# Kernel optimization log

Hardware: AMD Instinct MI355X
Metric: run time of the kernel (lower is better)

## Reference

```python
import jax, jax.numpy as jnp
import numpy as np

SCALE = 64.0
MARGIN = 0.35
EPS = 1e-12  # torch F.normalize eps


def _l2norm(a, axis):
    n = jnp.sqrt(jnp.sum(a * a, axis=axis, keepdims=True))
    return a / jnp.maximum(n, EPS)


def setup_inputs() -> dict:
    key = jax.random.key(0)
    k1, k2, k3 = jax.random.split(key, 3)
    B, D, C = 512, 512, 100000
    x = jax.random.normal(k1, (B, D), dtype=jnp.float32)
    gt = jax.random.randint(k2, (B,), 0, C, dtype=jnp.int64)
    # kaiming_normal_ on [C, D]: std = sqrt(2 / fan_in) with fan_in = D
    wt = jax.random.normal(k3, (C, D), dtype=jnp.float32) * np.sqrt(2.0 / D)
    return {"x": x, "gt": gt, "wt": wt}


def reference(x, gt, wt):
    wt_norm = _l2norm(wt, axis=1)          # [C, D]
    x_norm = _l2norm(x, axis=1)            # [B, D]
    cos = jnp.einsum("bd,cd->bc", x_norm, wt_norm)  # [B, C]
    # margin only at target index (avoids materializing one-hot)
    b = jnp.arange(x.shape[0])
    margin_score = cos.at[b, gt].add(-MARGIN)
    logits = SCALE * margin_score
    logp = jax.nn.log_softmax(logits, axis=-1)
    nll = -logp[b, gt]
    return jnp.mean(nll)
```

## Files before the change

kernel.cpp:

```cpp
#include <hip/hip_runtime.h>
#include <hip/hip_bf16.h>

#define DIM 512
#define BATCH 512
#define CCLS 100000
#define BN 128
#define NT 782

typedef __attribute__((ext_vector_type(4))) float f32x4;

__device__ __forceinline__ void async_copy16(const unsigned char* g, unsigned char* l) {
  __builtin_amdgcn_global_load_lds((const __attribute__((address_space(1))) void*)g,
                                   (__attribute__((address_space(3))) void*)l, 16, 0, 0);
}

__global__ __launch_bounds__(256) void xquant(const float* __restrict__ x,
                                              unsigned char* __restrict__ xq,
                                              float* __restrict__ nx) {
  int wave = threadIdx.x >> 6;
  int lane = threadIdx.x & 63;
  int row = blockIdx.x * 4 + wave;
  const float4* src = (const float4*)(x + (size_t)row * DIM);
  float4 v0 = src[2 * lane];
  float4 v1 = src[2 * lane + 1];
  float ss = v0.x*v0.x + v0.y*v0.y + v0.z*v0.z + v0.w*v0.w
           + v1.x*v1.x + v1.y*v1.y + v1.z*v1.z + v1.w*v1.w;
  #pragma unroll
  for (int off = 32; off > 0; off >>= 1) ss += __shfl_xor(ss, off, 64);
  int p0 = __builtin_amdgcn_cvt_pk_fp8_f32(v0.x, v0.y, 0, false);
  p0     = __builtin_amdgcn_cvt_pk_fp8_f32(v0.z, v0.w, p0, true);
  int p1 = __builtin_amdgcn_cvt_pk_fp8_f32(v1.x, v1.y, 0, false);
  p1     = __builtin_amdgcn_cvt_pk_fp8_f32(v1.z, v1.w, p1, true);
  ((int2*)(xq + (size_t)row * DIM))[lane] = make_int2(p0, p1);
  if (lane == 0) nx[row] = fmaxf(sqrtf(ss), 1e-12f);
}

__global__ __launch_bounds__(1024) void cosface_fused(
    const unsigned char* __restrict__ xq,
    const float* __restrict__ wt,
    const int* __restrict__ gt,
    const float* __restrict__ nx,
    float* __restrict__ partial,
    float* __restrict__ tgt) {
  __shared__ __align__(16) unsigned char lds_a[512 * 128];
  __shared__ __align__(16) unsigned char lds_b[BN * 128];
  __shared__ float lds_rowsum[BATCH];
  __shared__ float lds_nx[BATCH];
  __shared__ float lds_nw[BN];
  __shared__ int lds_gt[BATCH];

  const int tid = threadIdx.x;
  const int lane = tid & 63;
  const int w = tid >> 6;
  const int wm = w >> 2;
  const int wn_ = w & 3;
  const int nt = blockIdx.x;

  if (tid < BATCH) {
    lds_rowsum[tid] = 0.f;
    lds_gt[tid] = gt[tid];
    lds_nx[tid] = nx[tid];
  }
  if (tid < BN) lds_nw[tid] = 0.f;

  unsigned int oa[4];
  #pragma unroll
  for (int j = 0; j < 4; ++j) {
    int c = j * 1024 + tid;
    int m = c >> 3;
    int qg = (c & 7) ^ (m & 7);
    oa[j] = (unsigned int)m * DIM + qg * 16;
  }
  const int mB = tid >> 3;
  const int qgB = (tid & 7) ^ (mB & 7);
  int rowB = nt * BN + mB;
  if (rowB >= CCLS) rowB = CCLS - 1;
  const float* wsrc = wt + (size_t)rowB * DIM + qgB * 16;

  f32x4 acc[8][2];
  #pragma unroll
  for (int i = 0; i < 8; ++i)
    #pragma unroll
    for (int j = 0; j < 2; ++j)
      acc[i][j] = (f32x4){0.f, 0.f, 0.f, 0.f};

  const int quad = lane >> 4;
  const int l15 = lane & 15;
  const int sw = l15 & 7;
  __syncthreads();

  for (int kk = 0; kk < 4; ++kk) {
    #pragma unroll
    for (int j = 0; j < 4; ++j)
      async_copy16(xq + oa[j] + kk * 128, &lds_a[(j * 1024 + w * 64) * 16]);
    {
      const float* p = wsrc + kk * 128;
      float4 f0 = *(const float4*)(p);
      float4 f1 = *(const float4*)(p + 4);
      float4 f2 = *(const float4*)(p + 8);
      float4 f3 = *(const float4*)(p + 12);
      f0.x*=16.f; f0.y*=16.f; f0.z*=16.f; f0.w*=16.f;
      f1.x*=16.f; f1.y*=16.f; f1.z*=16.f; f1.w*=16.f;
      f2.x*=16.f; f2.y*=16.f; f2.z*=16.f; f2.w*=16.f;
      f3.x*=16.f; f3.y*=16.f; f3.z*=16.f; f3.w*=16.f;
      float ss = f0.x*f0.x + f0.y*f0.y + f0.z*f0.z + f0.w*f0.w
               + f1.x*f1.x + f1.y*f1.y + f1.z*f1.z + f1.w*f1.w
               + f2.x*f2.x + f2.y*f2.y + f2.z*f2.z + f2.w*f2.w
               + f3.x*f3.x + f3.y*f3.y + f3.z*f3.z + f3.w*f3.w;
      int p0 = __builtin_amdgcn_cvt_pk_fp8_f32(f0.x, f0.y, 0, false);
      p0     = __builtin_amdgcn_cvt_pk_fp8_f32(f0.z, f0.w, p0, true);
      int p1 = __builtin_amdgcn_cvt_pk_fp8_f32(f1.x, f1.y, 0, false);
      p1     = __builtin_amdgcn_cvt_pk_fp8_f32(f1.z, f1.w, p1, true);
      int p2 = __builtin_amdgcn_cvt_pk_fp8_f32(f2.x, f2.y, 0, false);
      p2     = __builtin_amdgcn_cvt_pk_fp8_f32(f2.z, f2.w, p2, true);
      int p3 = __builtin_amdgcn_cvt_pk_fp8_f32(f3.x, f3.y, 0, false);
      p3     = __builtin_amdgcn_cvt_pk_fp8_f32(f3.z, f3.w, p3, true);
      ((int4*)lds_b)[tid] = make_int4(p0, p1, p2, p3);
      ss += __shfl_xor(ss, 1, 64);
      ss += __shfl_xor(ss, 2, 64);
      ss += __shfl_xor(ss, 4, 64);
      if ((lane & 7) == 0) atomicAdd(&lds_nw[mB], ss);
    }
    __syncthreads();

    #pragma unroll
    for (int s = 0; s < 4; ++s) {
      int g = s * 4 + quad;
      int cs = g >> 1;
      int h = (g & 1) * 8;
      long long af[8], bf[2];
      #pragma unroll
      for (int i = 0; i < 8; ++i)
        af[i] = *(const long long*)&lds_a[(wm * 128 + i * 16 + l15) * 128 + ((cs ^ sw) * 16) + h];
      #pragma unroll
      for (int j = 0; j < 2; ++j)
        bf[j] = *(const long long*)&lds_b[(wn_ * 32 + j * 16 + l15) * 128 + ((cs ^ sw) * 16) + h];
      #pragma unroll
      for (int i = 0; i < 8; ++i)
        #pragma unroll
        for (int j = 0; j < 2; ++j)
          acc[i][j] = __builtin_amdgcn_mfma_f32_16x16x32_fp8_fp8(af[i], bf[j], acc[i][j], 0, 0, 0);
    }
    __syncthreads();
  }

  float rnw[2];
  #pragma unroll
  for (int j = 0; j < 2; ++j)
    rnw[j] = 1.0f / fmaxf(sqrtf(lds_nw[wn_ * 32 + j * 16 + l15]), 1e-12f);
  #pragma unroll
  for (int i = 0; i < 8; ++i) {
    #pragma unroll
    for (int reg = 0; reg < 4; ++reg) {
      int m_loc = wm * 128 + i * 16 + quad * 4 + reg;
      int gtm = lds_gt[m_loc];
      float rx = 64.0f / lds_nx[m_loc];
      float s = 0.f;
      #pragma unroll
      for (int j = 0; j < 2; ++j) {
        int n_g = nt * BN + wn_ * 32 + j * 16 + l15;
        float logit = acc[i][j][reg] * rnw[j] * rx;
        if (n_g == gtm) {
          logit -= 64.f * 0.35f;
          tgt[m_loc] = logit;
        }
        if (n_g < CCLS) s += __expf(logit - 64.f);
      }
      #pragma unroll
      for (int off = 1; off < 16; off <<= 1) s += __shfl_xor(s, off, 64);
      if (l15 == 0) atomicAdd(&lds_rowsum[m_loc], s);
    }
  }
  __syncthreads();
  if (tid < BATCH)
    partial[(size_t)tid * NT + nt] = lds_rowsum[tid];
}

__global__ __launch_bounds__(64) void nll_rows(const float* __restrict__ partial,
                                               const float* __restrict__ tgt,
                                               float* __restrict__ nll) {
  int m = blockIdx.x;
  int lane = threadIdx.x;
  const float* row = partial + (size_t)m * NT;
  float s = 0.f;
  for (int t = lane; t < NT; t += 64) s += row[t];
  #pragma unroll
  for (int off = 32; off > 0; off >>= 1) s += __shfl_xor(s, off, 64);
  if (lane == 0) nll[m] = (logf(s) + 64.f) - tgt[m];
}

__global__ __launch_bounds__(512) void reduce_mean(const float* __restrict__ nll,
                                                   float* __restrict__ out) {
  __shared__ float red[BATCH];
  int m = threadIdx.x;
  red[m] = nll[m];
  __syncthreads();
  for (int k = 256; k > 0; k >>= 1) {
    if (m < k) red[m] += red[m + k];
    __syncthreads();
  }
  if (m == 0) out[0] = red[0] * (1.0f / BATCH);
}

extern "C" void kernel_launch(void* const* d_in, const int* in_sizes, int n_in,
                              void* d_out, int out_size, void* d_ws, size_t ws_size,
                              hipStream_t stream) {
  const float* x  = (const float*)d_in[0];
  const int*   gt = (const int*)d_in[1];
  const float* wt = (const float*)d_in[2];
  float* out = (float*)d_out;

  char* ws = (char*)d_ws;
  unsigned char* xq = (unsigned char*)ws;
  float* nx         = (float*)(ws + 262144);
  float* partial    = (float*)(ws + 264192);
  float* tgt        = (float*)(ws + 1865728);
  float* nll        = (float*)(ws + 1867776);

  xquant<<<BATCH / 4, 256, 0, stream>>>(x, xq, nx);
  cosface_fused<<<NT, 1024, 0, stream>>>(xq, wt, gt, nx, partial, tgt);
  nll_rows<<<BATCH, 64, 0, stream>>>(partial, tgt, nll);
  reduce_mean<<<1, BATCH, 0, stream>>>(nll, out);
}
```

Before: 393.7 us.

## Double-buffer K loop with smaller class tiles and register-prefetched weight loads

Class tile width is halved to 64 with 512-thread blocks and a 4-blocks-per-SM launch bound. The K loop now walks 8 steps of 64 bytes with double-buffered LDS for both the fp8 x tile and the quantized weight tile, and global weight loads are prefetched two steps ahead in registers. The per-row weight norm is kept in registers and reduced once at the end, replacing per-step LDS atomics. This aims to overlap the HBM stream of the fp32 weights with MFMA work and raise occupancy. In exchange, the x tile is staged from L2 twice as often in total and the partial-sum array is twice as large.

```diff
diff --git a/kernel.cpp b/kernel.cpp
--- a/kernel.cpp
+++ b/kernel.cpp
@@ -4,8 +4,8 @@
 #define DIM 512
 #define BATCH 512
 #define CCLS 100000
-#define BN 128
-#define NT 782
+#define BN 64
+#define NT 1563
 
 typedef __attribute__((ext_vector_type(4))) float f32x4;
 
@@ -35,47 +35,70 @@
   if (lane == 0) nx[row] = fmaxf(sqrtf(ss), 1e-12f);
 }
 
-__global__ __launch_bounds__(1024) void cosface_fused(
+__global__ __launch_bounds__(512, 4) void cosface_fused(
     const unsigned char* __restrict__ xq,
     const float* __restrict__ wt,
     const int* __restrict__ gt,
     const float* __restrict__ nx,
     float* __restrict__ partial,
     float* __restrict__ tgt) {
-  __shared__ __align__(16) unsigned char lds_a[512 * 128];
-  __shared__ __align__(16) unsigned char lds_b[BN * 128];
-  __shared__ float lds_rowsum[BATCH];
-  __shared__ float lds_nx[BATCH];
+  __shared__ __align__(16) unsigned char lds_a[2][512 * 64];
+  __shared__ __align__(16) unsigned char lds_b[2][BN * 64];
+  __shared__ float lds_rowsum[512];
+  __shared__ float lds_nx[512];
   __shared__ float lds_nw[BN];
-  __shared__ int lds_gt[BATCH];
+  __shared__ int lds_gt[512];
 
   const int tid = threadIdx.x;
   const int lane = tid & 63;
   const int w = tid >> 6;
-  const int wm = w >> 2;
-  const int wn_ = w & 3;
+  const int wm = w >> 1;
+  const int wn_ = w & 1;
   const int nt = blockIdx.x;
 
-  if (tid < BATCH) {
-    lds_rowsum[tid] = 0.f;
-    lds_gt[tid] = gt[tid];
-    lds_nx[tid] = nx[tid];
-  }
-  if (tid < BN) lds_nw[tid] = 0.f;
+  lds_rowsum[tid] = 0.f;
+  lds_gt[tid] = gt[tid];
+  lds_nx[tid] = nx[tid];
 
   unsigned int oa[4];
   #pragma unroll
   for (int j = 0; j < 4; ++j) {
-    int c = j * 1024 + tid;
-    int m = c >> 3;
-    int qg = (c & 7) ^ (m & 7);
-    oa[j] = (unsigned int)m * DIM + qg * 16;
-  }
-  const int mB = tid >> 3;
-  const int qgB = (tid & 7) ^ (mB & 7);
-  int rowB = nt * BN + mB;
+    int c = j * 512 + tid;
+    int m = c >> 2;
+    int qc = (c & 3) ^ ((m >> 1) & 3);
+    oa[j] = (unsigned int)m * DIM + qc * 16;
+  }
+#define STAGEA(sel, kk) do {                                                 \
+    _Pragma("unroll")                                                        \
+    for (int j = 0; j < 4; ++j)                                              \
+      async_copy16(xq + oa[j] + (kk) * 64,                                   \
+                   &lds_a[sel][(j * 512 + w * 64) * 16]);                    \
+  } while (0)
+
+  const int r0 = tid >> 3;
+  const int g0 = tid & 7;
+  int rowB = nt * BN + r0;
   if (rowB >= CCLS) rowB = CCLS - 1;
-  const float* wsrc = wt + (size_t)rowB * DIM + qgB * 16;
+  const float* wsrc = wt + (size_t)rowB * DIM + g0 * 8;
+  const int pb_off = r0 * 64 + (g0 ^ (((r0 >> 1) & 3) << 1)) * 8;
+
+#define LOADB(K) do {                                                        \
+    const float* p_ = wsrc + (K) * 64;                                       \
+    f0 = *(const float4*)(p_);                                               \
+    f1 = *(const float4*)(p_ + 4);                                           \
+  } while (0)
+
+#define QUANT8() do {                                                        \
+    f0.x*=16.f; f0.y*=16.f; f0.z*=16.f; f0.w*=16.f;                          \
+    f1.x*=16.f; f1.y*=16.f; f1.z*=16.f; f1.w*=16.f;                          \
+    ssq += f0.x*f0.x + f0.y*f0.y + f0.z*f0.z + f0.w*f0.w                     \
+         + f1.x*f1.x + f1.y*f1.y + f1.z*f1.z + f1.w*f1.w;                    \
+    int q0_ = __builtin_amdgcn_cvt_pk_fp8_f32(f0.x, f0.y, 0, false);         \
+    q0_     = __builtin_amdgcn_cvt_pk_fp8_f32(f0.z, f0.w, q0_, true);        \
+    int q1_ = __builtin_amdgcn_cvt_pk_fp8_f32(f1.x, f1.y, 0, false);         \
+    q1_     = __builtin_amdgcn_cvt_pk_fp8_f32(f1.z, f1.w, q1_, true);        \
+    pq = make_int2(q0_, q1_);                                                \
+  } while (0)
 
   f32x4 acc[8][2];
   #pragma unroll
@@ -86,63 +109,55 @@
 
   const int quad = lane >> 4;
   const int l15 = lane & 15;
-  const int sw = l15 & 7;
-  __syncthreads();
-
-  for (int kk = 0; kk < 4; ++kk) {
+  const int swg = ((l15 >> 1) & 3) << 1;
+  float4 f0, f1;
+  int2 pq;
+  float ssq = 0.f;
+
+  STAGEA(0, 0);
+  LOADB(0); QUANT8();
+  *(int2*)&lds_b[0][pb_off] = pq;
+  LOADB(1); QUANT8();
+  __syncthreads();
+
+  #pragma unroll
+  for (int kk = 0; kk < 8; ++kk) {
+    const int cur = kk & 1;
+    if (kk < 7) {
+      *(int2*)&lds_b[cur ^ 1][pb_off] = pq;
+      STAGEA(cur ^ 1, kk + 1);
+    }
+    if (kk < 6) LOADB(kk + 2);
+
     #pragma unroll
-    for (int j = 0; j < 4; ++j)
-      async_copy16(xq + oa[j] + kk * 128, &lds_a[(j * 1024 + w * 64) * 16]);
-    {
-      const float* p = wsrc + kk * 128;
-      float4 f0 = *(const float4*)(p);
-      float4 f1 = *(const float4*)(p + 4);
-      float4 f2 = *(const float4*)(p + 8);
-      float4 f3 = *(const float4*)(p + 12);
-      f0.x*=16.f; f0.y*=16.f; f0.z*=16.f; f0.w*=16.f;
-      f1.x*=16.f; f1.y*=16.f; f1.z*=16.f; f1.w*=16.f;
-      f2.x*=16.f; f2.y*=16.f; f2.z*=16.f; f2.w*=16.f;
-      f3.x*=16.f; f3.y*=16.f; f3.z*=16.f; f3.w*=16.f;
-      float ss = f0.x*f0.x + f0.y*f0.y + f0.z*f0.z + f0.w*f0.w
-               + f1.x*f1.x + f1.y*f1.y + f1.z*f1.z + f1.w*f1.w
-               + f2.x*f2.x + f2.y*f2.y + f2.z*f2.z + f2.w*f2.w
-               + f3.x*f3.x + f3.y*f3.y + f3.z*f3.z + f3.w*f3.w;
-      int p0 = __builtin_amdgcn_cvt_pk_fp8_f32(f0.x, f0.y, 0, false);
-      p0     = __builtin_amdgcn_cvt_pk_fp8_f32(f0.z, f0.w, p0, true);
-      int p1 = __builtin_amdgcn_cvt_pk_fp8_f32(f1.x, f1.y, 0, false);
-      p1     = __builtin_amdgcn_cvt_pk_fp8_f32(f1.z, f1.w, p1, true);
-      int p2 = __builtin_amdgcn_cvt_pk_fp8_f32(f2.x, f2.y, 0, false);
-      p2     = __builtin_amdgcn_cvt_pk_fp8_f32(f2.z, f2.w, p2, true);
-      int p3 = __builtin_amdgcn_cvt_pk_fp8_f32(f3.x, f3.y, 0, false);
-      p3     = __builtin_amdgcn_cvt_pk_fp8_f32(f3.z, f3.w, p3, true);
-      ((int4*)lds_b)[tid] = make_int4(p0, p1, p2, p3);
-      ss += __shfl_xor(ss, 1, 64);
-      ss += __shfl_xor(ss, 2, 64);
-      ss += __shfl_xor(ss, 4, 64);
-      if ((lane & 7) == 0) atomicAdd(&lds_nw[mB], ss);
-    }
-    __syncthreads();
-
-    #pragma unroll
-    for (int s = 0; s < 4; ++s) {
-      int g = s * 4 + quad;
-      int cs = g >> 1;
-      int h = (g & 1) * 8;
+    for (int s = 0; s < 2; ++s) {
+      const int off = (((s * 4 + quad) ^ swg) << 3);
       long long af[8], bf[2];
       #pragma unroll
       for (int i = 0; i < 8; ++i)
-        af[i] = *(const long long*)&lds_a[(wm * 128 + i * 16 + l15) * 128 + ((cs ^ sw) * 16) + h];
+        af[i] = *(const long long*)&lds_a[cur][(wm * 128 + i * 16 + l15) * 64 + off];
       #pragma unroll
       for (int j = 0; j < 2; ++j)
-        bf[j] = *(const long long*)&lds_b[(wn_ * 32 + j * 16 + l15) * 128 + ((cs ^ sw) * 16) + h];
+        bf[j] = *(const long long*)&lds_b[cur][(wn_ * 32 + j * 16 + l15) * 64 + off];
       #pragma unroll
       for (int i = 0; i < 8; ++i)
         #pragma unroll
         for (int j = 0; j < 2; ++j)
           acc[i][j] = __builtin_amdgcn_mfma_f32_16x16x32_fp8_fp8(af[i], bf[j], acc[i][j], 0, 0, 0);
     }
-    __syncthreads();
-  }
+
+    if (kk < 6) QUANT8();
+    if (kk < 7) __syncthreads();
+  }
+#undef STAGEA
+#undef LOADB
+#undef QUANT8
+
+  ssq += __shfl_xor(ssq, 1, 64);
+  ssq += __shfl_xor(ssq, 2, 64);
+  ssq += __shfl_xor(ssq, 4, 64);
+  if ((lane & 7) == 0) lds_nw[r0] = ssq;
+  __syncthreads();
 
   float rnw[2];
   #pragma unroll
@@ -172,8 +187,7 @@
     }
   }
   __syncthreads();
-  if (tid < BATCH)
-    partial[(size_t)tid * NT + nt] = lds_rowsum[tid];
+  partial[(size_t)tid * NT + nt] = lds_rowsum[tid];
 }
 
 __global__ __launch_bounds__(64) void nll_rows(const float* __restrict__ partial,
@@ -214,11 +228,11 @@
   unsigned char* xq = (unsigned char*)ws;
   float* nx         = (float*)(ws + 262144);
   float* partial    = (float*)(ws + 264192);
-  float* tgt        = (float*)(ws + 1865728);
-  float* nll        = (float*)(ws + 1867776);
+  float* tgt        = (float*)(ws + 3465216);
+  float* nll        = (float*)(ws + 3467264);
 
   xquant<<<BATCH / 4, 256, 0, stream>>>(x, xq, nx);
-  cosface_fused<<<NT, 1024, 0, stream>>>(xq, wt, gt, nx, partial, tgt);
+  cosface_fused<<<NT, 512, 0, stream>>>(xq, wt, gt, nx, partial, tgt);
   nll_rows<<<BATCH, 64, 0, stream>>>(partial, tgt, nll);
   reduce_mean<<<1, BATCH, 0, stream>>>(nll, out);
 }
```

Measured after the change: 363.3 us. 1.08x faster.
